# Performance work log

Measured on AMD Instinct MI355X. Metric: run time of the kernel, lower is better.

Reference implementation:

```python
import jax, jax.numpy as jnp
import numpy as np

B, T, D, E, H, F, K = 4, 2048, 2048, 16, 1024, 1024, 2


def setup_inputs() -> dict:
    key = jax.random.key(0)
    ks = jax.random.split(key, 7)
    sD, sH, sF = D ** -0.5, H ** -0.5, F ** -0.5
    hidden_state = jax.random.normal(ks[0], (B, T, D), jnp.float32)
    Wr = jax.random.normal(ks[1], (D, E), jnp.float32) * sD      # router
    Wg = jax.random.normal(ks[2], (D, 1), jnp.float32) * sD      # shared gate
    W1 = jax.random.normal(ks[3], (E, D, H), jnp.float32) * sD   # expert up-proj
    W2 = jax.random.normal(ks[4], (E, H, D), jnp.float32) * sH   # expert down-proj
    W1s = jax.random.normal(ks[5], (D, F), jnp.float32) * sD     # shared expert up
    W2s = jax.random.normal(ks[6], (F, D), jnp.float32) * sF     # shared expert down
    return {"hidden_state": hidden_state, "Wr": Wr, "Wg": Wg,
            "W1": W1, "W2": W2, "W1s": W1s, "W2s": W2s}


def reference(hidden_state, Wr, Wg, W1, W2, W1s, W2s):
    b, t, d = hidden_state.shape
    N = b * t
    x = hidden_state.reshape(N, d)

    # Router: softmax scores + shared-expert sigmoid gate
    s = jax.nn.softmax(x @ Wr, axis=-1)           # [N, E]
    g_shared = jax.nn.sigmoid(x @ Wg)             # [N, 1]

    topk_vals, topk_idx = jax.lax.top_k(s, K)     # [N, K]

    # Dense combine weights: gate[n,e] = topk_vals if expert e chosen, else 0.
    # Mathematically identical to sort/gather/scatter-add dispatch in the source.
    gate = jnp.zeros((N, E), dtype=s.dtype).at[
        jnp.arange(N)[:, None], topk_idx].add(topk_vals)

    # Per-expert FFN (fixed small expert loop), gate-weighted combine
    y = jnp.zeros_like(x)
    for e in range(E):
        h = jax.nn.gelu(x @ W1[e], approximate=False)   # [N, H]
        y = y + gate[:, e:e + 1] * (h @ W2[e])

    # Shared expert, scaled by sigmoid gate
    shared = jax.nn.gelu(x @ W1s, approximate=False) @ W2s
    y = y + g_shared * shared
    y_out = y.reshape(b, t, d)

    # Aux stats (attention_mask is None branch)
    importance = s.mean(axis=0)                               # [E]
    counts = jnp.zeros((E,), jnp.float32).at[topk_idx.reshape(-1)].add(1.0)
    load = counts / (counts.sum() + 1e-12)
    return y_out, importance, load
```

## Files before the change

kernel.cpp:

```cpp
#include <hip/hip_runtime.h>
#include <hip/hip_bf16.h>


#define N_TOK 8192
#define DDIM  2048
#define NEXP  16
#define HDIM  1024
#define FDIM  1024
#define NASSIGN (N_TOK * 2)
#define NROWS (NASSIGN + N_TOK)

typedef __attribute__((ext_vector_type(8))) short bf16x8;
typedef __attribute__((ext_vector_type(4))) float f32x4;
typedef __attribute__((ext_vector_type(8))) unsigned short u16x8;
typedef __attribute__((ext_vector_type(4))) unsigned short u16x4;

__device__ inline unsigned short f2bf(float f) {
    unsigned int u = __builtin_bit_cast(unsigned int, f);
    u += 0x7FFFu + ((u >> 16) & 1u);
    return (unsigned short)(u >> 16);
}

__device__ inline float bf2f(unsigned short h) {
    return __builtin_bit_cast(float, (unsigned int)h << 16);
}

__device__ inline float gelu_f(float v) {
    return 0.5f * v * (1.0f + erff(v * 0.7071067811865475f));
}

__device__ inline void gld16(void* lds, const void* g) {
    __builtin_amdgcn_global_load_lds(
        (const __attribute__((address_space(1))) unsigned int*)g,
        (__attribute__((address_space(3))) unsigned int*)lds, 16, 0, 0);
}

__global__ __launch_bounds__(256) void zero_small(float* imp) {
    if (threadIdx.x < NEXP) imp[threadIdx.x] = 0.0f;
}

__global__ __launch_bounds__(256) void cast_x_kernel(const float* __restrict__ x,
                                                     unsigned short* __restrict__ xb) {
    size_t i = (size_t)blockIdx.x * 256 + threadIdx.x;
    const float4 a = ((const float4*)x)[i * 2];
    const float4 b = ((const float4*)x)[i * 2 + 1];
    u16x8 o;
    o[0] = f2bf(a.x); o[1] = f2bf(a.y); o[2] = f2bf(a.z); o[3] = f2bf(a.w);
    o[4] = f2bf(b.x); o[5] = f2bf(b.y); o[6] = f2bf(b.z); o[7] = f2bf(b.w);
    *(u16x8*)(xb + i * 8) = o;
}

template <int R, int C>
__global__ __launch_bounds__(256) void transpose_cast(const float* __restrict__ src,
                                                      unsigned short* __restrict__ dst) {
    __shared__ unsigned short t[64][66];
    const size_t zoff = (size_t)blockIdx.z * R * C;
    src += zoff; dst += zoff;
    const int r0 = blockIdx.y * 64, c0 = blockIdx.x * 64;
    const int tid = threadIdx.x;
    const int cr = tid >> 4;
    const int cc4 = (tid & 15) * 4;
#pragma unroll
    for (int it = 0; it < 4; ++it) {
        int row = cr + it * 16;
        const float4 v = *(const float4*)(src + (size_t)(r0 + row) * C + c0 + cc4);
        t[row][cc4 + 0] = f2bf(v.x); t[row][cc4 + 1] = f2bf(v.y);
        t[row][cc4 + 2] = f2bf(v.z); t[row][cc4 + 3] = f2bf(v.w);
    }
    __syncthreads();
#pragma unroll
    for (int it = 0; it < 4; ++it) {
        int cc = cr + it * 16;
        u16x4 o;
#pragma unroll
        for (int j = 0; j < 4; ++j) o[j] = t[cc4 + j][cc];
        *(u16x4*)(dst + (size_t)(c0 + cc) * R + r0 + cc4) = o;
    }
}

__global__ __launch_bounds__(256) void router_kernel(
    const float* __restrict__ x, const float* __restrict__ Wr, const float* __restrict__ Wg,
    float* __restrict__ gsh, int* __restrict__ t2i, float* __restrict__ t2v,
    float* __restrict__ imp) {
    __shared__ float simp[NEXP];
    const int tid = threadIdx.x, lane = tid & 63, w = tid >> 6;
    if (tid < NEXP) simp[tid] = 0.0f;
    __syncthreads();
    const int n = blockIdx.x * 4 + w;
    const float* xr = x + (size_t)n * DDIM;
    float acc[NEXP];
#pragma unroll
    for (int e = 0; e < NEXP; ++e) acc[e] = 0.0f;
    float ag = 0.0f;
    for (int j = 0; j < DDIM / 64; ++j) {
        int d = lane + j * 64;
        float xv = xr[d];
        const float* wr = Wr + (size_t)d * NEXP;
#pragma unroll
        for (int e = 0; e < NEXP; ++e) acc[e] = fmaf(xv, wr[e], acc[e]);
        ag = fmaf(xv, Wg[d], ag);
    }
#pragma unroll
    for (int off = 32; off; off >>= 1) {
#pragma unroll
        for (int e = 0; e < NEXP; ++e) acc[e] += __shfl_xor(acc[e], off);
        ag += __shfl_xor(ag, off);
    }
    if (lane == 0) {
        float mx = acc[0];
#pragma unroll
        for (int e = 1; e < NEXP; ++e) mx = fmaxf(mx, acc[e]);
        float p[NEXP], s = 0.0f;
#pragma unroll
        for (int e = 0; e < NEXP; ++e) { p[e] = expf(acc[e] - mx); s += p[e]; }
        const float inv = 1.0f / s;
        int i1 = 0; float v1 = -1.0f;
#pragma unroll
        for (int e = 0; e < NEXP; ++e) {
            p[e] *= inv;
            if (p[e] > v1) { v1 = p[e]; i1 = e; }
        }
        int i2 = 0; float v2 = -1.0f;
#pragma unroll
        for (int e = 0; e < NEXP; ++e) {
            if (e != i1 && p[e] > v2) { v2 = p[e]; i2 = e; }
        }
        t2i[2 * n] = i1; t2i[2 * n + 1] = i2;
        t2v[2 * n] = v1; t2v[2 * n + 1] = v2;
        gsh[n] = 1.0f / (1.0f + expf(-ag));
#pragma unroll
        for (int e = 0; e < NEXP; ++e) atomicAdd(&simp[e], p[e]);
    }
    __syncthreads();
    if (tid < NEXP) unsafeAtomicAdd(&imp[tid], simp[tid]);
}

__global__ __launch_bounds__(256) void scan_finalize(
    const int* __restrict__ t2i, const float* __restrict__ imp,
    int* __restrict__ offs, int* __restrict__ fill, float* __restrict__ out_tail) {
    __shared__ int hist[NEXP];
    const int tid = threadIdx.x;
    if (tid < NEXP) hist[tid] = 0;
    __syncthreads();
    for (int i = tid; i < NASSIGN; i += 256) atomicAdd(&hist[t2i[i]], 1);
    __syncthreads();
    if (tid == 0) {
        int o = 0;
        for (int e = 0; e < NEXP; ++e) { offs[e] = o; o += hist[e]; }
        offs[NEXP] = o;
        offs[NEXP + 1] = NROWS;
    }
    if (tid < NEXP) {
        fill[tid] = 0;
        out_tail[tid] = imp[tid] * (1.0f / (float)N_TOK);
        out_tail[NEXP + tid] = (float)hist[tid] / (float)NASSIGN;
    }
}

__global__ __launch_bounds__(256) void build_assign(
    const int* __restrict__ t2i, const float* __restrict__ t2v,
    const int* __restrict__ offs, int* __restrict__ fill,
    int* __restrict__ atok, float* __restrict__ agate, int* __restrict__ t2pos) {
    const int n = blockIdx.x * 256 + threadIdx.x;
#pragma unroll
    for (int k = 0; k < 2; ++k) {
        int e = t2i[2 * n + k];
        int pos = offs[e] + atomicAdd(&fill[e], 1);
        atok[pos] = n;
        agate[pos] = t2v[2 * n + k];
        t2pos[2 * n + k] = pos;
    }
    atok[NASSIGN + n] = n;
    agate[NASSIGN + n] = 1.0f;
}

__global__ __launch_bounds__(256) void combine_kernel(
    const unsigned short* __restrict__ contrib, const int* __restrict__ t2pos,
    const float* __restrict__ gsh, float* __restrict__ y) {
    const int gi = blockIdx.x * 256 + threadIdx.x;
    const int n = gi >> 8;
    const int d8 = (gi & 255) * 8;
    const int p0 = t2pos[2 * n], p1 = t2pos[2 * n + 1];
    const float g = gsh[n];
    u16x8 a = *(const u16x8*)(contrib + (size_t)p0 * DDIM + d8);
    u16x8 b = *(const u16x8*)(contrib + (size_t)p1 * DDIM + d8);
    u16x8 c = *(const u16x8*)(contrib + (size_t)(NASSIGN + n) * DDIM + d8);
    float4 y0, y1;
    y0.x = bf2f(a[0]) + bf2f(b[0]) + g * bf2f(c[0]);
    y0.y = bf2f(a[1]) + bf2f(b[1]) + g * bf2f(c[1]);
    y0.z = bf2f(a[2]) + bf2f(b[2]) + g * bf2f(c[2]);
    y0.w = bf2f(a[3]) + bf2f(b[3]) + g * bf2f(c[3]);
    y1.x = bf2f(a[4]) + bf2f(b[4]) + g * bf2f(c[4]);
    y1.y = bf2f(a[5]) + bf2f(b[5]) + g * bf2f(c[5]);
    y1.z = bf2f(a[6]) + bf2f(b[6]) + g * bf2f(c[6]);
    y1.w = bf2f(a[7]) + bf2f(b[7]) + g * bf2f(c[7]);
    float* yr = y + (size_t)n * DDIM + d8;
    *(float4*)yr = y0;
    *(float4*)(yr + 4) = y1;
}

#define BAR()   __builtin_amdgcn_s_barrier()
#define WAITL() do { asm volatile("s_waitcnt lgkmcnt(0)" ::: "memory"); \
                     __builtin_amdgcn_sched_barrier(0); } while (0)

#define RD_A(dst, mb) do {                                                  \
  _Pragma("unroll") for (int i_ = 0; i_ < 4; ++i_)                          \
  _Pragma("unroll") for (int kh_ = 0; kh_ < 2; ++kh_)                       \
    (dst)[i_][kh_] = *(const bf16x8*)(aB + rbA[kh_] + ((mb) + i_) * 2048);  \
} while (0)

#define RD_B(dst, nb) do {                                                  \
  _Pragma("unroll") for (int i_ = 0; i_ < 2; ++i_)                          \
  _Pragma("unroll") for (int kh_ = 0; kh_ < 2; ++kh_)                       \
    (dst)[i_][kh_] = *(const bf16x8*)(bB + rbB[kh_] + ((nb) + i_) * 2048);  \
} while (0)

#define MM(mb, nb, a_, b_) do {                                             \
  __builtin_amdgcn_s_setprio(1);                                            \
  _Pragma("unroll") for (int i_ = 0; i_ < 4; ++i_)                          \
  _Pragma("unroll") for (int n_ = 0; n_ < 2; ++n_)                          \
  _Pragma("unroll") for (int kh_ = 0; kh_ < 2; ++kh_)                       \
    acc[(mb) + i_][(nb) + n_] = __builtin_amdgcn_mfma_f32_16x16x32_bf16(    \
        (a_)[i_][kh_], (b_)[n_][kh_], acc[(mb) + i_][(nb) + n_], 0, 0, 0);  \
  __builtin_amdgcn_s_setprio(0);                                            \
} while (0)

#define STG(dstbuf, src, kt) do {                                           \
    gld16((char*)(dstbuf) + ldso0, (src)[0] + (size_t)(kt) * 64);           \
    gld16((char*)(dstbuf) + ldso1, (src)[1] + (size_t)(kt) * 64);           \
} while (0)

#define KTILE(d, t) do {                                                    \
    const char* aB = (const char*)As_[d][wm];                               \
    const char* bB = (const char*)Bs_[d][bh];                               \
    const int ka = ((t) + 1 < NT) ? (t) + 1 : (t);                          \
    const int kb = ((t) + 2 < NT) ? (t) + 2 : (t);                          \
    bf16x8 av[4][2], bv0[2][2], bv1[2][2];                                  \
    RD_A(av, 0); RD_B(bv0, 0);                                              \
    STG(As_[(d) ^ 1][0], sA[0], ka);                                        \
    BAR(); WAITL();                                                         \
    MM(0, 0, av, bv0);                                                      \
    BAR();                                                                  \
    RD_B(bv1, 2);                                                           \
    STG(As_[(d) ^ 1][1], sA[1], ka);                                        \
    BAR(); WAITL();                                                         \
    MM(0, 2, av, bv1);                                                      \
    BAR();                                                                  \
    RD_A(av, 4);                                                            \
    STG(Bs_[d][0], sB[0], kb);                                              \
    BAR(); WAITL();                                                         \
    MM(4, 0, av, bv0);                                                      \
    BAR();                                                                  \
    STG(Bs_[d][1], sB[1], kb);                                              \
    BAR();                                                                  \
    MM(4, 2, av, bv1);                                                      \
    asm volatile("s_waitcnt vmcnt(4)" ::: "memory");                        \
    BAR();                                                                  \
} while (0)

template <int MODE>
__global__ __launch_bounds__(512, 2) void gemm8(
    const unsigned short* __restrict__ A, const unsigned short* __restrict__ B,
    unsigned short* __restrict__ out,
    const int* __restrict__ offs, const int* __restrict__ atok,
    const float* __restrict__ agate) {
    constexpr int KD = MODE == 0 ? DDIM : HDIM;
    constexpr int NC = MODE == 0 ? HDIM : DDIM;
    constexpr int NT = KD / 64;
    const int e = blockIdx.z;
    const int m0 = offs[e];
    const int mE = offs[e + 1] - m0;
    const int tm = blockIdx.y;
    if (tm * 256 >= mE) return;
    const int n0 = blockIdx.x * 256;

    __shared__ __align__(16) unsigned short As_[2][2][128 * 64];
    __shared__ __align__(16) unsigned short Bs_[2][2][128 * 64];

    const int tid = threadIdx.x;
    const int lane = tid & 63, w = tid >> 6;
    const int wm = w >> 2, wn = w & 3;
    const int bh = wn >> 1;

    const int kch = ((lane & 7) ^ ((lane >> 3) & 7)) * 8;
    const int ldso0 = (w * 128 + lane) * 16;
    const int ldso1 = (w * 128 + 64 + lane) * 16;
    const unsigned short* sA[2][2];
    const unsigned short* sB[2][2];
#pragma unroll
    for (int h = 0; h < 2; ++h) {
#pragma unroll
        for (int j = 0; j < 2; ++j) {
            int rr = h * 128 + w * 16 + j * 8 + (lane >> 3);
            int ar = tm * 256 + rr; ar = ar < mE ? ar : mE - 1;
            if (MODE == 0)
                sA[h][j] = A + (size_t)atok[m0 + ar] * KD + kch;
            else
                sA[h][j] = A + (size_t)(m0 + ar) * KD + kch;
            sB[h][j] = B + (size_t)e * KD * NC + (size_t)(n0 + rr) * KD + kch;
        }
    }

    const int c16 = lane & 15, q = lane >> 4;
    int rbA[2], rbB[2];
#pragma unroll
    for (int kh = 0; kh < 2; ++kh) {
        int sl = (kh * 4 + q) ^ (c16 & 7);
        rbA[kh] = c16 * 128 + sl * 16;
        rbB[kh] = ((wn & 1) * 64 + c16) * 128 + sl * 16;
    }

    f32x4 acc[8][4];
#pragma unroll
    for (int i = 0; i < 8; ++i)
#pragma unroll
        for (int j = 0; j < 4; ++j) acc[i][j] = (f32x4){0.f, 0.f, 0.f, 0.f};

    STG(As_[0][0], sA[0], 0); STG(As_[0][1], sA[1], 0);
    STG(Bs_[0][0], sB[0], 0); STG(Bs_[0][1], sB[1], 0);
    STG(Bs_[1][0], sB[0], 1); STG(Bs_[1][1], sB[1], 1);
    asm volatile("s_waitcnt vmcnt(4)" ::: "memory");
    BAR();

#pragma unroll 1
    for (int it = 0; it < NT / 2; ++it) {
        const int t0 = it * 2;
        KTILE(0, t0);
        KTILE(1, t0 + 1);
    }

    const int col = lane & 15, r4 = (lane >> 4) * 4;
#pragma unroll
    for (int mi = 0; mi < 8; ++mi) {
#pragma unroll
        for (int r = 0; r < 4; ++r) {
            int grow = tm * 256 + wm * 128 + mi * 16 + r4 + r;
            if (grow >= mE) continue;
            float gate = (MODE == 0) ? agate[m0 + grow] : 0.0f;
#pragma unroll
            for (int ni = 0; ni < 4; ++ni) {
                int gcol = n0 + wn * 64 + ni * 16 + col;
                float v = acc[mi][ni][r];
                if (MODE == 0)
                    out[(size_t)(m0 + grow) * NC + gcol] = f2bf(gelu_f(v) * gate);
                else
                    out[(size_t)(m0 + grow) * NC + gcol] = f2bf(v);
            }
        }
    }
}

extern "C" void kernel_launch(void* const* d_in, const int* in_sizes, int n_in,
                              void* d_out, int out_size, void* d_ws, size_t ws_size,
                              hipStream_t stream) {
    const float* x   = (const float*)d_in[0];
    const float* Wr  = (const float*)d_in[1];
    const float* Wg  = (const float*)d_in[2];
    const float* W1  = (const float*)d_in[3];
    const float* W2  = (const float*)d_in[4];
    const float* W1s = (const float*)d_in[5];
    const float* W2s = (const float*)d_in[6];
    float* out = (float*)d_out;

    char* ws = (char*)d_ws;
    size_t off = 0;
    auto carve = [&](size_t bytes) { char* p = ws + off; off += (bytes + 255) & ~(size_t)255; return p; };
    unsigned short* xb    = (unsigned short*)carve((size_t)N_TOK * DDIM * 2);
    unsigned short* w1all = (unsigned short*)carve((size_t)(NEXP + 1) * DDIM * HDIM * 2);
    unsigned short* w2all = (unsigned short*)carve((size_t)(NEXP + 1) * HDIM * DDIM * 2);
    unsigned short* hb    = (unsigned short*)carve((size_t)NROWS * HDIM * 2);
    float* gsh            = (float*)carve((size_t)N_TOK * 4);
    int* t2i              = (int*)carve((size_t)N_TOK * 2 * 4);
    float* t2v            = (float*)carve((size_t)N_TOK * 2 * 4);
    int* atok             = (int*)carve((size_t)NROWS * 4);
    float* agate          = (float*)carve((size_t)NROWS * 4);
    int* t2pos            = (int*)carve((size_t)NASSIGN * 4);
    float* imp            = (float*)carve(256);
    int* offs             = (int*)carve(256);
    int* fill             = (int*)carve(256);
    if (ws_size < off) return;

    unsigned short* contrib = (unsigned short*)ws;

    float* out_tail = out + (size_t)N_TOK * DDIM;

    hipLaunchKernelGGL(zero_small, dim3(1), dim3(256), 0, stream, imp);
    hipLaunchKernelGGL(cast_x_kernel, dim3(N_TOK * DDIM / 8 / 256), dim3(256), 0, stream, x, xb);
    hipLaunchKernelGGL((transpose_cast<DDIM, HDIM>), dim3(HDIM / 64, DDIM / 64, NEXP), dim3(256), 0, stream, W1, w1all);
    hipLaunchKernelGGL((transpose_cast<DDIM, HDIM>), dim3(HDIM / 64, DDIM / 64, 1), dim3(256), 0, stream,
                       W1s, w1all + (size_t)NEXP * DDIM * HDIM);
    hipLaunchKernelGGL((transpose_cast<HDIM, DDIM>), dim3(DDIM / 64, HDIM / 64, NEXP), dim3(256), 0, stream, W2, w2all);
    hipLaunchKernelGGL((transpose_cast<HDIM, DDIM>), dim3(DDIM / 64, HDIM / 64, 1), dim3(256), 0, stream,
                       W2s, w2all + (size_t)NEXP * HDIM * DDIM);
    hipLaunchKernelGGL(router_kernel, dim3(N_TOK / 4), dim3(256), 0, stream, x, Wr, Wg, gsh, t2i, t2v, imp);
    hipLaunchKernelGGL(scan_finalize, dim3(1), dim3(256), 0, stream, t2i, imp, offs, fill, out_tail);
    hipLaunchKernelGGL(build_assign, dim3(N_TOK / 256), dim3(256), 0, stream, t2i, t2v, offs, fill, atok, agate, t2pos);

    hipLaunchKernelGGL((gemm8<0>), dim3(HDIM / 256, N_TOK / 256, NEXP + 1), dim3(512), 0, stream,
                       xb, w1all, hb, offs, atok, agate);
    hipLaunchKernelGGL((gemm8<1>), dim3(DDIM / 256, N_TOK / 256, NEXP + 1), dim3(512), 0, stream,
                       hb, w2all, contrib, offs, atok, agate);
    hipLaunchKernelGGL(combine_kernel, dim3(N_TOK * DDIM / 8 / 256), dim3(256), 0, stream,
                       contrib, t2pos, gsh, out);
}
```

Baseline: 724.3 us.

## Replace 8-phase GEMM pipeline with simple 2-stage K=32 double-buffered loop

Swaps the hand-interleaved 8-phase MFMA/LDS/global-load schedule for a simpler double-buffered loop over K in steps of 32, using smaller LDS tiles (256x32 per operand per buffer). Launch bounds are raised to request 4 blocks per CU instead of 2. The aim is more occupancy and less barrier and scheduling overhead. The cost is fewer MFMAs per barrier, less overlap of loads with compute, and heavy register pressure from the 8x4 accumulator array under the tighter launch bound.

```diff
diff --git a/kernel.cpp b/kernel.cpp
--- a/kernel.cpp
+++ b/kernel.cpp
@@ -199,74 +199,14 @@
     *(float4*)(yr + 4) = y1;
 }
 
-#define BAR()   __builtin_amdgcn_s_barrier()
-#define WAITL() do { asm volatile("s_waitcnt lgkmcnt(0)" ::: "memory"); \
-                     __builtin_amdgcn_sched_barrier(0); } while (0)
-
-#define RD_A(dst, mb) do {                                                  \
-  _Pragma("unroll") for (int i_ = 0; i_ < 4; ++i_)                          \
-  _Pragma("unroll") for (int kh_ = 0; kh_ < 2; ++kh_)                       \
-    (dst)[i_][kh_] = *(const bf16x8*)(aB + rbA[kh_] + ((mb) + i_) * 2048);  \
-} while (0)
-
-#define RD_B(dst, nb) do {                                                  \
-  _Pragma("unroll") for (int i_ = 0; i_ < 2; ++i_)                          \
-  _Pragma("unroll") for (int kh_ = 0; kh_ < 2; ++kh_)                       \
-    (dst)[i_][kh_] = *(const bf16x8*)(bB + rbB[kh_] + ((nb) + i_) * 2048);  \
-} while (0)
-
-#define MM(mb, nb, a_, b_) do {                                             \
-  __builtin_amdgcn_s_setprio(1);                                            \
-  _Pragma("unroll") for (int i_ = 0; i_ < 4; ++i_)                          \
-  _Pragma("unroll") for (int n_ = 0; n_ < 2; ++n_)                          \
-  _Pragma("unroll") for (int kh_ = 0; kh_ < 2; ++kh_)                       \
-    acc[(mb) + i_][(nb) + n_] = __builtin_amdgcn_mfma_f32_16x16x32_bf16(    \
-        (a_)[i_][kh_], (b_)[n_][kh_], acc[(mb) + i_][(nb) + n_], 0, 0, 0);  \
-  __builtin_amdgcn_s_setprio(0);                                            \
-} while (0)
-
-#define STG(dstbuf, src, kt) do {                                           \
-    gld16((char*)(dstbuf) + ldso0, (src)[0] + (size_t)(kt) * 64);           \
-    gld16((char*)(dstbuf) + ldso1, (src)[1] + (size_t)(kt) * 64);           \
-} while (0)
-
-#define KTILE(d, t) do {                                                    \
-    const char* aB = (const char*)As_[d][wm];                               \
-    const char* bB = (const char*)Bs_[d][bh];                               \
-    const int ka = ((t) + 1 < NT) ? (t) + 1 : (t);                          \
-    const int kb = ((t) + 2 < NT) ? (t) + 2 : (t);                          \
-    bf16x8 av[4][2], bv0[2][2], bv1[2][2];                                  \
-    RD_A(av, 0); RD_B(bv0, 0);                                              \
-    STG(As_[(d) ^ 1][0], sA[0], ka);                                        \
-    BAR(); WAITL();                                                         \
-    MM(0, 0, av, bv0);                                                      \
-    BAR();                                                                  \
-    RD_B(bv1, 2);                                                           \
-    STG(As_[(d) ^ 1][1], sA[1], ka);                                        \
-    BAR(); WAITL();                                                         \
-    MM(0, 2, av, bv1);                                                      \
-    BAR();                                                                  \
-    RD_A(av, 4);                                                            \
-    STG(Bs_[d][0], sB[0], kb);                                              \
-    BAR(); WAITL();                                                         \
-    MM(4, 0, av, bv0);                                                      \
-    BAR();                                                                  \
-    STG(Bs_[d][1], sB[1], kb);                                              \
-    BAR();                                                                  \
-    MM(4, 2, av, bv1);                                                      \
-    asm volatile("s_waitcnt vmcnt(4)" ::: "memory");                        \
-    BAR();                                                                  \
-} while (0)
-
 template <int MODE>
-__global__ __launch_bounds__(512, 2) void gemm8(
+__global__ __launch_bounds__(512, 4) void gemm2p(
     const unsigned short* __restrict__ A, const unsigned short* __restrict__ B,
     unsigned short* __restrict__ out,
     const int* __restrict__ offs, const int* __restrict__ atok,
     const float* __restrict__ agate) {
     constexpr int KD = MODE == 0 ? DDIM : HDIM;
     constexpr int NC = MODE == 0 ? HDIM : DDIM;
-    constexpr int NT = KD / 64;
     const int e = blockIdx.z;
     const int m0 = offs[e];
     const int mE = offs[e + 1] - m0;
@@ -274,59 +214,72 @@
     if (tm * 256 >= mE) return;
     const int n0 = blockIdx.x * 256;
 
-    __shared__ __align__(16) unsigned short As_[2][2][128 * 64];
-    __shared__ __align__(16) unsigned short Bs_[2][2][128 * 64];
+    __shared__ __align__(16) unsigned short As_[2][256 * 32];
+    __shared__ __align__(16) unsigned short Bs_[2][256 * 32];
 
     const int tid = threadIdx.x;
     const int lane = tid & 63, w = tid >> 6;
     const int wm = w >> 2, wn = w & 3;
-    const int bh = wn >> 1;
-
-    const int kch = ((lane & 7) ^ ((lane >> 3) & 7)) * 8;
-    const int ldso0 = (w * 128 + lane) * 16;
-    const int ldso1 = (w * 128 + 64 + lane) * 16;
-    const unsigned short* sA[2][2];
-    const unsigned short* sB[2][2];
-#pragma unroll
-    for (int h = 0; h < 2; ++h) {
-#pragma unroll
-        for (int j = 0; j < 2; ++j) {
-            int rr = h * 128 + w * 16 + j * 8 + (lane >> 3);
-            int ar = tm * 256 + rr; ar = ar < mE ? ar : mE - 1;
-            if (MODE == 0)
-                sA[h][j] = A + (size_t)atok[m0 + ar] * KD + kch;
-            else
-                sA[h][j] = A + (size_t)(m0 + ar) * KD + kch;
-            sB[h][j] = B + (size_t)e * KD * NC + (size_t)(n0 + rr) * KD + kch;
-        }
-    }
-
-    const int c16 = lane & 15, q = lane >> 4;
-    int rbA[2], rbB[2];
-#pragma unroll
-    for (int kh = 0; kh < 2; ++kh) {
-        int sl = (kh * 4 + q) ^ (c16 & 7);
-        rbA[kh] = c16 * 128 + sl * 16;
-        rbB[kh] = ((wn & 1) * 64 + c16) * 128 + sl * 16;
-    }
-
-    f32x4 acc[8][4];
-#pragma unroll
-    for (int i = 0; i < 8; ++i)
-#pragma unroll
-        for (int j = 0; j < 4; ++j) acc[i][j] = (f32x4){0.f, 0.f, 0.f, 0.f};
-
-    STG(As_[0][0], sA[0], 0); STG(As_[0][1], sA[1], 0);
-    STG(Bs_[0][0], sB[0], 0); STG(Bs_[0][1], sB[1], 0);
-    STG(Bs_[1][0], sB[0], 1); STG(Bs_[1][1], sB[1], 1);
-    asm volatile("s_waitcnt vmcnt(4)" ::: "memory");
-    BAR();
+
+    const unsigned short* sA[2];
+    const unsigned short* sB[2];
+    int dOff[2];
+#pragma unroll
+    for (int it = 0; it < 2; ++it) {
+        int c = tid + it * 512;
+        int row = c >> 2, slot = c & 3;
+        int ksw = (slot ^ ((row >> 1) & 3)) * 8;
+        int arow = tm * 256 + row; arow = arow < mE ? arow : mE - 1;
+        if (MODE == 0)
+            sA[it] = A + (size_t)atok[m0 + arow] * KD + ksw;
+        else
+            sA[it] = A + (size_t)(m0 + arow) * KD + ksw;
+        sB[it] = B + (size_t)e * KD * NC + (size_t)(n0 + row) * KD + ksw;
+        dOff[it] = c * 16;
+    }
+
+    f32x4 acc[8][4] = {};
+
+    auto stage = [&](int b, int kk) {
+        gld16((char*)As_[b] + dOff[0], sA[0] + kk);
+        gld16((char*)As_[b] + dOff[1], sA[1] + kk);
+        gld16((char*)Bs_[b] + dOff[0], sB[0] + kk);
+        gld16((char*)Bs_[b] + dOff[1], sB[1] + kk);
+    };
+    auto compute = [&](int b) {
+        const int c16 = lane & 15, q = lane >> 4;
+        bf16x8 av[8], bv[4];
+#pragma unroll
+        for (int mi = 0; mi < 8; ++mi) {
+            int r = wm * 128 + mi * 16 + c16;
+            int s = q ^ ((r >> 1) & 3);
+            av[mi] = *(const bf16x8*)((const char*)As_[b] + r * 64 + s * 16);
+        }
+#pragma unroll
+        for (int ni = 0; ni < 4; ++ni) {
+            int r = wn * 64 + ni * 16 + c16;
+            int s = q ^ ((r >> 1) & 3);
+            bv[ni] = *(const bf16x8*)((const char*)Bs_[b] + r * 64 + s * 16);
+        }
+#pragma unroll
+        for (int mi = 0; mi < 8; ++mi)
+#pragma unroll
+            for (int ni = 0; ni < 4; ++ni)
+                acc[mi][ni] = __builtin_amdgcn_mfma_f32_16x16x32_bf16(
+                    av[mi], bv[ni], acc[mi][ni], 0, 0, 0);
+    };
+
+    stage(0, 0);
+    __syncthreads();
 
 #pragma unroll 1
-    for (int it = 0; it < NT / 2; ++it) {
-        const int t0 = it * 2;
-        KTILE(0, t0);
-        KTILE(1, t0 + 1);
+    for (int kk = 0; kk < KD; kk += 64) {
+        stage(1, kk + 32);
+        compute(0);
+        __syncthreads();
+        if (kk + 64 < KD) stage(0, kk + 64);
+        compute(1);
+        __syncthreads();
     }
 
     const int col = lane & 15, r4 = (lane >> 4) * 4;
@@ -396,9 +349,9 @@
     hipLaunchKernelGGL(scan_finalize, dim3(1), dim3(256), 0, stream, t2i, imp, offs, fill, out_tail);
     hipLaunchKernelGGL(build_assign, dim3(N_TOK / 256), dim3(256), 0, stream, t2i, t2v, offs, fill, atok, agate, t2pos);
 
-    hipLaunchKernelGGL((gemm8<0>), dim3(HDIM / 256, N_TOK / 256, NEXP + 1), dim3(512), 0, stream,
+    hipLaunchKernelGGL((gemm2p<0>), dim3(HDIM / 256, N_TOK / 256, NEXP + 1), dim3(512), 0, stream,
                        xb, w1all, hb, offs, atok, agate);
-    hipLaunchKernelGGL((gemm8<1>), dim3(DDIM / 256, N_TOK / 256, NEXP + 1), dim3(512), 0, stream,
+    hipLaunchKernelGGL((gemm2p<1>), dim3(DDIM / 256, N_TOK / 256, NEXP + 1), dim3(512), 0, stream,
                        hb, w2all, contrib, offs, atok, agate);
     hipLaunchKernelGGL(combine_kernel, dim3(N_TOK * DDIM / 8 / 256), dim3(256), 0, stream,
                        contrib, t2pos, gsh, out);
```

Result: slower. 2.445 ms (+237.6%).
